# Optimization experiments

Measured on AMD Instinct MI355X. Metric: run time of the kernel, lower is better.

The kernel has to match this reference:

```python
import jax, jax.numpy as jnp
import numpy as np

N = 100000
E = 1600000
IN_CH = 128
HID = 16
HEADS = 4
OUT_CH = 2
EDGE_DIM = 3
NEG_SLOPE = 0.2


def gat_layer(x, src, dst, e_feat, W, att_src, att_dst, We, att_edge, bias, H, C, concat):
    # x: [N, Fin] -> projected [N, H, C]
    xs = (x @ W).reshape(-1, H, C)
    a_src = jnp.sum(xs * att_src, axis=-1)          # [N, H]
    a_dst = jnp.sum(xs * att_dst, axis=-1)          # [N, H]
    ee = (e_feat @ We).reshape(-1, H, C)            # [E, H, C]
    a_edge = jnp.sum(ee * att_edge, axis=-1)        # [E, H]
    alpha = a_src[src] + a_dst[dst] + a_edge        # [E, H]
    alpha = jax.nn.leaky_relu(alpha, NEG_SLOPE)
    # segment softmax over incoming edges of each dst node
    seg_max = jax.ops.segment_max(alpha, dst, num_segments=N)
    alpha = jnp.exp(alpha - seg_max[dst])
    seg_sum = jax.ops.segment_sum(alpha, dst, num_segments=N)
    alpha = alpha / (seg_sum[dst] + 1e-16)
    # weighted message aggregation
    msg = xs[src] * alpha[:, :, None]               # [E, H, C]
    out = jax.ops.segment_sum(msg, dst, num_segments=N)  # [N, H, C]
    out = out.reshape(-1, H * C) if concat else out.mean(axis=1)
    return out + bias


def setup_inputs() -> dict:
    key = jax.random.key(0)
    ks = jax.random.split(key, 24)
    g = lambda i, shape, scale=0.1: jax.random.normal(ks[i], shape, dtype=jnp.float32) * scale
    inp = {
        "x": jax.random.normal(ks[0], (N, IN_CH), dtype=jnp.float32),
        "edge_index": jax.random.randint(ks[1], (2, E), 0, N, dtype=jnp.int32),
        "edge_feat": jax.random.normal(ks[2], (E, EDGE_DIM), dtype=jnp.float32),
        # edge MLP
        "Em1": g(3, (EDGE_DIM, EDGE_DIM)), "eb1": g(4, (EDGE_DIM,)),
        "Em2": g(5, (EDGE_DIM, EDGE_DIM)), "eb2": g(6, (EDGE_DIM,)),
        # conv1: in -> HID per head, HEADS heads, concat
        "W1": g(7, (IN_CH, HEADS * HID)),
        "as1": g(8, (HEADS, HID)), "ad1": g(9, (HEADS, HID)),
        "We1": g(10, (EDGE_DIM, HEADS * HID)), "ae1": g(11, (HEADS, HID)),
        "b1": g(12, (HEADS * HID,)),
        # conv2: HEADS*HID -> OUT_CH, 1 head, no concat
        "W2": g(13, (HEADS * HID, OUT_CH)),
        "as2": g(14, (1, OUT_CH)), "ad2": g(15, (1, OUT_CH)),
        "We2": g(16, (EDGE_DIM, OUT_CH)), "ae2": g(17, (1, OUT_CH)),
        "b2": g(18, (OUT_CH,)),
    }
    return inp


def reference(x, edge_index, edge_feat,
              Em1, eb1, Em2, eb2,
              W1, as1, ad1, We1, ae1, b1,
              W2, as2, ad2, We2, ae2, b2):
    src, dst = edge_index[0], edge_index[1]
    # edge MLP: Linear -> ReLU -> Linear
    e = jax.nn.relu(edge_feat @ Em1 + eb1) @ Em2 + eb2
    # dropout layers are identity in eval mode
    h = gat_layer(x, src, dst, e, W1, as1, ad1, We1, ae1, b1, HEADS, HID, concat=True)
    h = jax.nn.elu(h)
    out = gat_layer(h, src, dst, e, W2, as2, ad2, We2, ae2, b2, 1, OUT_CH, concat=False)
    return out
```

## Files before the change

### kernel.cpp

```cpp
#include <hip/hip_runtime.h>
#include <hip/hip_fp16.h>
#include <math.h>
#include <stdint.h>

#define NEG_SLOPE 0.2f
#define SCAN_TILE 2048

__device__ __forceinline__ float leaky(float a) { return a > 0.f ? a : NEG_SLOPE * a; }

__global__ __launch_bounds__(256) void k_pw(const int* __restrict__ dst, int* __restrict__ deg,
                                            int* __restrict__ pw, int E,
                                            const float* __restrict__ We1, const float* __restrict__ ae1,
                                            const float* __restrict__ We2, const float* __restrict__ ae2,
                                            float* __restrict__ cw) {
    if (blockIdx.x == 0 && threadIdx.x == 0) {
        for (int i = 0; i < 3; i++)
            for (int h = 0; h < 4; h++) {
                float s = 0.f;
                for (int m = 0; m < 16; m++) s += We1[i*64 + h*16 + m] * ae1[h*16 + m];
                cw[i*4 + h] = s;
            }
        for (int i = 0; i < 3; i++) cw[12 + i] = We2[i*2]*ae2[0] + We2[i*2+1]*ae2[1];
    }
    int base = (blockIdx.x * blockDim.x + threadIdx.x) * 4;
    if (base >= E) return;
    if (base + 3 < E) {
        int4 dv = *reinterpret_cast<const int4*>(&dst[base]);
        int4 pv;
        pv.x = atomicAdd(&deg[dv.x], 1);
        pv.y = atomicAdd(&deg[dv.y], 1);
        pv.z = atomicAdd(&deg[dv.z], 1);
        pv.w = atomicAdd(&deg[dv.w], 1);
        *reinterpret_cast<int4*>(&pw[base]) = pv;
    } else {
        for (int i = base; i < E; i++) pw[i] = atomicAdd(&deg[dst[i]], 1);
    }
}

__global__ __launch_bounds__(256) void k_scan_partial(const int* __restrict__ deg, int* __restrict__ tsum, int N) {
    __shared__ int sh[256];
    int b = blockIdx.x, t = threadIdx.x;
    int base = b * SCAN_TILE + t * 8;
    int s = 0;
    #pragma unroll
    for (int i = 0; i < 8; i++) { int idx = base + i; s += (idx < N) ? deg[idx] : 0; }
    sh[t] = s; __syncthreads();
    for (int o = 128; o > 0; o >>= 1) { if (t < o) sh[t] += sh[t + o]; __syncthreads(); }
    if (t == 0) tsum[b] = sh[0];
}

__global__ void k_scan_tsum(const int* __restrict__ tsum, int* __restrict__ toff,
                            int* __restrict__ rowptr, int nb, int N) {
    if (threadIdx.x == 0 && blockIdx.x == 0) {
        int run = 0;
        for (int i = 0; i < nb; i++) { toff[i] = run; run += tsum[i]; }
        rowptr[N] = run;
    }
}

__global__ __launch_bounds__(256) void k_scan_final(const int* __restrict__ deg, const int* __restrict__ toff,
        int* __restrict__ rowptr, int* __restrict__ cmbi, int N) {
    __shared__ int sh[256];
    int b = blockIdx.x, t = threadIdx.x;
    int base = b * SCAN_TILE + t * 8;
    int v[8]; int s = 0;
    #pragma unroll
    for (int i = 0; i < 8; i++) { int idx = base + i; v[i] = (idx < N) ? deg[idx] : 0; s += v[i]; }
    sh[t] = s; __syncthreads();
    for (int o = 1; o < 256; o <<= 1) {
        int u = (t >= o) ? sh[t - o] : 0;
        __syncthreads();
        sh[t] += u;
        __syncthreads();
    }
    int run = sh[t] - s + toff[b];
    #pragma unroll
    for (int i = 0; i < 8; i++) {
        int idx = base + i;
        if (idx < N) { rowptr[idx] = run; cmbi[(size_t)idx*8 + 4] = run; run += v[i]; }
    }
}

__global__ __launch_bounds__(256) void k_proj1(const float* __restrict__ x, const float* __restrict__ W1,
        const float* __restrict__ as1, const float* __restrict__ ad1,
        __half* __restrict__ xs1h, float* __restrict__ as1v, float* __restrict__ cmbf, int N) {
    __shared__ float xr[32][128];
    int tid = threadIdx.x;
    int wave = tid >> 6, lane = tid & 63;
    int nbase = blockIdx.x * 32;
    if (nbase + 32 <= N) {
        const float4* x4 = reinterpret_cast<const float4*>(x + (size_t)nbase * 128);
        #pragma unroll
        for (int i = 0; i < 4; i++) {
            int idx = tid + i * 256;
            reinterpret_cast<float4*>(&xr[0][0])[idx] = x4[idx];
        }
    } else {
        for (int i = 0; i < 16; i++) {
            int flat = tid + i * 256;
            int row = flat >> 7, col = flat & 127;
            int n = nbase + row; if (n >= N) n = N - 1;
            xr[row][col] = x[(size_t)n * 128 + col];
        }
    }
    __syncthreads();
    int cc = lane & 15, kk = lane >> 4;
    int nw = wave * 8;
    const float4* W4 = reinterpret_cast<const float4*>(W1);
    float4 acc[8];
    #pragma unroll
    for (int m = 0; m < 8; m++) acc[m] = make_float4(0.f, 0.f, 0.f, 0.f);
    #pragma unroll 4
    for (int k = kk; k < 128; k += 4) {
        float4 wv = W4[k * 16 + cc];
        #pragma unroll
        for (int m = 0; m < 8; m++) {
            float xv = xr[nw + m][k];
            acc[m].x = fmaf(xv, wv.x, acc[m].x);
            acc[m].y = fmaf(xv, wv.y, acc[m].y);
            acc[m].z = fmaf(xv, wv.z, acc[m].z);
            acc[m].w = fmaf(xv, wv.w, acc[m].w);
        }
    }
    float a_s0 = as1[4*cc], a_s1 = as1[4*cc+1], a_s2 = as1[4*cc+2], a_s3 = as1[4*cc+3];
    float a_d0 = ad1[4*cc], a_d1 = ad1[4*cc+1], a_d2 = ad1[4*cc+2], a_d3 = ad1[4*cc+3];
    #pragma unroll
    for (int m = 0; m < 8; m++) {
        float4 a = acc[m];
        a.x += __shfl_xor(a.x, 16, 64); a.y += __shfl_xor(a.y, 16, 64);
        a.z += __shfl_xor(a.z, 16, 64); a.w += __shfl_xor(a.w, 16, 64);
        a.x += __shfl_xor(a.x, 32, 64); a.y += __shfl_xor(a.y, 32, 64);
        a.z += __shfl_xor(a.z, 32, 64); a.w += __shfl_xor(a.w, 32, 64);
        float ps = a.x*a_s0 + a.y*a_s1 + a.z*a_s2 + a.w*a_s3;
        float pd = a.x*a_d0 + a.y*a_d1 + a.z*a_d2 + a.w*a_d3;
        ps += __shfl_xor(ps, 1, 64); ps += __shfl_xor(ps, 2, 64);
        pd += __shfl_xor(pd, 1, 64); pd += __shfl_xor(pd, 2, 64);
        if (kk == 0) {
            int n = nbase + nw + m; if (n >= N) n = N - 1;
            __half2 h01 = __halves2half2(__float2half_rn(a.x), __float2half_rn(a.y));
            __half2 h23 = __halves2half2(__float2half_rn(a.z), __float2half_rn(a.w));
            uint2 st;
            st.x = *reinterpret_cast<unsigned*>(&h01);
            st.y = *reinterpret_cast<unsigned*>(&h23);
            *reinterpret_cast<uint2*>(&xs1h[(size_t)n*64 + 4*cc]) = st;
            if ((cc & 3) == 0) {
                int h = cc >> 2;
                as1v[n*4 + h] = ps;
                cmbf[(size_t)n*8 + h] = pd;
            }
        }
    }
}

__global__ __launch_bounds__(256) void k_payload(const float* __restrict__ ef,
                       const float* __restrict__ Em1, const float* __restrict__ eb1,
                       const float* __restrict__ Em2, const float* __restrict__ eb2,
                       const float* __restrict__ cw,
                       const int* __restrict__ src, const int* __restrict__ dst,
                       const int* __restrict__ pw,
                       const float4* __restrict__ as1v4,
                       const float* __restrict__ cmbf, const int* __restrict__ cmbi,
                       uint4* __restrict__ csr_pk, int E) {
    int base = (blockIdx.x * blockDim.x + threadIdx.x) * 4;
    if (base >= E) return;
    int cnt = min(4, E - base);

    float f[4][3]; int sv[4], dv[4], pv[4];
    if (cnt == 4) {
        const float4* ef4 = reinterpret_cast<const float4*>(ef);
        float4 a = ef4[base*3/4 + 0], b = ef4[base*3/4 + 1], c = ef4[base*3/4 + 2];
        f[0][0]=a.x; f[0][1]=a.y; f[0][2]=a.z;
        f[1][0]=a.w; f[1][1]=b.x; f[1][2]=b.y;
        f[2][0]=b.z; f[2][1]=b.w; f[2][2]=c.x;
        f[3][0]=c.y; f[3][1]=c.z; f[3][2]=c.w;
        int4 s4 = *reinterpret_cast<const int4*>(&src[base]);
        int4 d4 = *reinterpret_cast<const int4*>(&dst[base]);
        int4 p4 = *reinterpret_cast<const int4*>(&pw[base]);
        sv[0]=s4.x; sv[1]=s4.y; sv[2]=s4.z; sv[3]=s4.w;
        dv[0]=d4.x; dv[1]=d4.y; dv[2]=d4.z; dv[3]=d4.w;
        pv[0]=p4.x; pv[1]=p4.y; pv[2]=p4.z; pv[3]=p4.w;
    } else {
        for (int i = 0; i < cnt; i++) {
            f[i][0]=ef[(base+i)*3+0]; f[i][1]=ef[(base+i)*3+1]; f[i][2]=ef[(base+i)*3+2];
            sv[i]=src[base+i]; dv[i]=dst[base+i]; pv[i]=pw[base+i];
        }
    }

    #pragma unroll
    for (int i = 0; i < 4; i++) {
        if (i >= cnt) break;
        float f0=f[i][0], f1=f[i][1], f2=f[i][2];
        float t0 = fmaxf(f0*Em1[0]+f1*Em1[3]+f2*Em1[6]+eb1[0], 0.f);
        float t1 = fmaxf(f0*Em1[1]+f1*Em1[4]+f2*Em1[7]+eb1[1], 0.f);
        float t2 = fmaxf(f0*Em1[2]+f1*Em1[5]+f2*Em1[8]+eb1[2], 0.f);
        float u0 = t0*Em2[0]+t1*Em2[3]+t2*Em2[6]+eb2[0];
        float u1 = t0*Em2[1]+t1*Em2[4]+t2*Em2[7]+eb2[1];
        float u2 = t0*Em2[2]+t1*Em2[5]+t2*Em2[8]+eb2[2];
        int s = sv[i], d = dv[i];
        float4 av = as1v4[s];
        float4 bv = *reinterpret_cast<const float4*>(&cmbf[(size_t)d*8]);
        int rp = cmbi[(size_t)d*8 + 4];
        float w0 = __expf(leaky(av.x + bv.x + u0*cw[0] + u1*cw[4] + u2*cw[8]));
        float w1 = __expf(leaky(av.y + bv.y + u0*cw[1] + u1*cw[5] + u2*cw[9]));
        float w2 = __expf(leaky(av.z + bv.z + u0*cw[2] + u1*cw[6] + u2*cw[10]));
        float w3 = __expf(leaky(av.w + bv.w + u0*cw[3] + u1*cw[7] + u2*cw[11]));
        float e2 = u0*cw[12] + u1*cw[13] + u2*cw[14];
        __half2 lo = __halves2half2(__float2half_rn(w0), __float2half_rn(w1));
        __half2 hi = __halves2half2(__float2half_rn(w2), __float2half_rn(w3));
        uint4 pki;
        pki.x = (unsigned)s;
        pki.y = *reinterpret_cast<unsigned*>(&lo);
        pki.z = *reinterpret_cast<unsigned*>(&hi);
        pki.w = *reinterpret_cast<unsigned*>(&e2);
        csr_pk[rp + pv[i]] = pki;
    }
}

__global__ __launch_bounds__(256) void k_gat1(
        const int* __restrict__ rowptr, const uint4* __restrict__ csr_pk,
        const __half* __restrict__ xs1h,
        const float* __restrict__ b1, const float* __restrict__ W2,
        const float* __restrict__ as2, const float* __restrict__ ad2,
        float2* __restrict__ pk2, float* __restrict__ ad2v, int N) {
    int wave = threadIdx.x >> 6, lane = threadIdx.x & 63;
    int d = blockIdx.x * 4 + wave;
    if (d >= N) return;
    int beg = rowptr[d], end = rowptr[d+1];
    int jj = lane >> 2, hh = lane & 3;
    int k = lane, hk = lane >> 4;
    float smacc = 0.f, acc = 0.f;
    for (int off = beg; off < end; off += 16) {
        int j = off + jj;
        float w = 0.f; int s = 0;
        if (j < end) {
            uint4 p = csr_pk[j];
            s = (int)p.x;
            unsigned wb = (hh < 2) ? p.y : p.z;
            __half2 h2 = *reinterpret_cast<__half2*>(&wb);
            w = (hh & 1) ? __high2float(h2) : __low2float(h2);
        }
        smacc += w;
        if (end - off >= 16) {
            #pragma unroll
            for (int t = 0; t < 16; ++t) {
                float wt = __shfl(w, t*4 + hk, 64);
                int st   = __shfl(s, t*4, 64);
                acc = fmaf(wt, __half2float(xs1h[(size_t)st*64 + k]), acc);
            }
        } else {
            int lim = end - off;
            for (int t = 0; t < lim; ++t) {
                float wt = __shfl(w, t*4 + hk, 64);
                int st   = __shfl(s, t*4, 64);
                acc = fmaf(wt, __half2float(xs1h[(size_t)st*64 + k]), acc);
            }
        }
    }
    smacc += __shfl_xor(smacc, 4, 64);
    smacc += __shfl_xor(smacc, 8, 64);
    smacc += __shfl_xor(smacc, 16, 64);
    smacc += __shfl_xor(smacc, 32, 64);
    float sm = __shfl(smacc, hk, 64);
    float h = acc / (sm + 1e-16f);
    float v = h + b1[k];
    v = v > 0.f ? v : expm1f(v);
    float p0 = v * W2[k*2 + 0], p1 = v * W2[k*2 + 1];
    #pragma unroll
    for (int o = 32; o >= 1; o >>= 1) { p0 += __shfl_xor(p0,o,64); p1 += __shfl_xor(p1,o,64); }
    if (lane == 0) {
        float2 q;
        q.x = p0*as2[0] + p1*as2[1];
        __half2 xv = __halves2half2(__float2half_rn(p0), __float2half_rn(p1));
        q.y = *reinterpret_cast<float*>(&xv);
        pk2[d] = q;
        ad2v[d] = p0*ad2[0] + p1*ad2[1];
    }
}

__global__ __launch_bounds__(256) void k_gat2(
        const int* __restrict__ rowptr, const uint4* __restrict__ csr_pk,
        const float2* __restrict__ pk2, const float* __restrict__ ad2v,
        const float* __restrict__ b2, float* __restrict__ out, int N) {
    int t = blockIdx.x * blockDim.x + threadIdx.x;
    int d = t >> 4, j16 = t & 15;
    if (d >= N) return;
    int beg = rowptr[d], end = rowptr[d+1];
    float add = ad2v[d];
    float sm = 0.f, p0 = 0.f, p1 = 0.f;
    for (int off = beg; off < end; off += 16) {
        int j = off + j16;
        if (j < end) {
            uint4 p = csr_pk[j];
            int s = (int)p.x;
            float ea2 = *reinterpret_cast<float*>(&p.w);
            float2 q = pk2[s];
            float w = __expf(leaky(q.x + add + ea2));
            __half2 xv = *reinterpret_cast<__half2*>(&q.y);
            p0 = fmaf(w, __low2float(xv), p0);
            p1 = fmaf(w, __high2float(xv), p1);
            sm += w;
        }
    }
    #pragma unroll
    for (int o = 1; o < 16; o <<= 1) {
        sm += __shfl_xor(sm, o, 16);
        p0 += __shfl_xor(p0, o, 16);
        p1 += __shfl_xor(p1, o, 16);
    }
    if (j16 == 0) {
        float inv = 1.f / (sm + 1e-16f);
        out[d*2+0] = p0*inv + b2[0];
        out[d*2+1] = p1*inv + b2[1];
    }
}

extern "C" void kernel_launch(void* const* d_in, const int* in_sizes, int n_in,
                              void* d_out, int out_size, void* d_ws, size_t ws_size,
                              hipStream_t stream) {
    const float* x   = (const float*)d_in[0];
    const int*   ei  = (const int*)d_in[1];
    const float* ef  = (const float*)d_in[2];
    const float* Em1 = (const float*)d_in[3];
    const float* eb1 = (const float*)d_in[4];
    const float* Em2 = (const float*)d_in[5];
    const float* eb2 = (const float*)d_in[6];
    const float* W1  = (const float*)d_in[7];
    const float* as1 = (const float*)d_in[8];
    const float* ad1 = (const float*)d_in[9];
    const float* We1 = (const float*)d_in[10];
    const float* ae1 = (const float*)d_in[11];
    const float* b1  = (const float*)d_in[12];
    const float* W2  = (const float*)d_in[13];
    const float* as2 = (const float*)d_in[14];
    const float* ad2 = (const float*)d_in[15];
    const float* We2 = (const float*)d_in[16];
    const float* ae2 = (const float*)d_in[17];
    const float* b2  = (const float*)d_in[18];

    const int N = in_sizes[0] / 128;
    const int E = in_sizes[1] / 2;
    const int* srcp = ei;
    const int* dstp = ei + E;

    uintptr_t w = (uintptr_t)d_ws;
    auto alloc = [&](size_t bytes) -> void* {
        uintptr_t p = w; w += (bytes + 255) & ~(size_t)255; return (void*)p;
    };
    const int nb = (N + SCAN_TILE - 1) / SCAN_TILE;
    int*    deg     = (int*)alloc((size_t)N * sizeof(int));
    int*    rowptr  = (int*)alloc(((size_t)N + 1) * sizeof(int));
    int*    tsum    = (int*)alloc((size_t)nb * sizeof(int));
    int*    toff    = (int*)alloc((size_t)(nb + 1) * sizeof(int));
    float*  cw      = (float*)alloc(16 * sizeof(float));
    int*    pw      = (int*)alloc((size_t)E * sizeof(int));
    uint4*  csr_pk  = (uint4*)alloc((size_t)E * sizeof(uint4));
    __half* xs1h    = (__half*)alloc((size_t)N * 64 * sizeof(__half));
    float*  as1v    = (float*)alloc((size_t)N * 4 * sizeof(float));
    float*  cmb     = (float*)alloc((size_t)N * 8 * sizeof(float));
    float2* pk2     = (float2*)alloc((size_t)N * sizeof(float2));
    float*  ad2v    = (float*)alloc((size_t)N * sizeof(float));

    const int B = 256;

    hipMemsetAsync(deg, 0, (size_t)N * sizeof(int), stream);
    k_pw<<<(E/4+B-1)/B + 1, B, 0, stream>>>(dstp, deg, pw, E, We1, ae1, We2, ae2, cw);
    k_scan_partial<<<nb, 256, 0, stream>>>(deg, tsum, N);
    k_scan_tsum<<<1, 64, 0, stream>>>(tsum, toff, rowptr, nb, N);
    k_scan_final<<<nb, 256, 0, stream>>>(deg, toff, rowptr, (int*)cmb, N);
    k_proj1<<<(N+31)/32, 256, 0, stream>>>(x, W1, as1, ad1, xs1h, as1v, cmb, N);
    k_payload<<<(E/4+B-1)/B + 1, B, 0, stream>>>(ef, Em1, eb1, Em2, eb2, cw,
                                                 srcp, dstp, pw, (const float4*)as1v,
                                                 cmb, (const int*)cmb, csr_pk, E);
    k_gat1<<<(N+3)/4, 256, 0, stream>>>(rowptr, csr_pk, xs1h, b1, W2, as2, ad2, pk2, ad2v, N);
    k_gat2<<<(N*16+B-1)/B, B, 0, stream>>>(rowptr, csr_pk, pk2, ad2v, b2, (float*)d_out, N);
}
```

Baseline: 276.0 us.

## Restructure GAT layer-1 aggregation to process four edges per wave with vectorized gathers

The layer-1 aggregation kernel is remapped so each wave splits into four 16-lane groups. Each group handles a different edge, and each lane gathers four fp16 channels with an 8-byte load, where before every lane loaded a single channel per edge. Partial sums are then combined across the groups with cross-lane shuffles, and the softmax denominator is reduced within 16-lane segments. This is meant to cut per-edge load instruction count and serial shuffle overhead, and it adds a launch-bounds occupancy hint. The cost is extra shuffles per chunk and higher register pressure.

```diff
diff --git a/kernel.cpp b/kernel.cpp
--- a/kernel.cpp
+++ b/kernel.cpp
@@ -7,6 +7,7 @@
 #define SCAN_TILE 2048
 
 __device__ __forceinline__ float leaky(float a) { return a > 0.f ? a : NEG_SLOPE * a; }
+__device__ __forceinline__ __half2 u2h2(unsigned u) { return *reinterpret_cast<__half2*>(&u); }
 
 __global__ __launch_bounds__(256) void k_pw(const int* __restrict__ dst, int* __restrict__ deg,
                                             int* __restrict__ pw, int E,
@@ -216,7 +217,7 @@
     }
 }
 
-__global__ __launch_bounds__(256) void k_gat1(
+__global__ __launch_bounds__(256, 4) void k_gat1(
         const int* __restrict__ rowptr, const uint4* __restrict__ csr_pk,
         const __half* __restrict__ xs1h,
         const float* __restrict__ b1, const float* __restrict__ W2,
@@ -226,47 +227,78 @@
     int d = blockIdx.x * 4 + wave;
     if (d >= N) return;
     int beg = rowptr[d], end = rowptr[d+1];
-    int jj = lane >> 2, hh = lane & 3;
-    int k = lane, hk = lane >> 4;
-    float smacc = 0.f, acc = 0.f;
+    int cg = lane & 15, e4 = lane >> 4;
+    int hh = cg >> 2;
+    const __half* xbase = xs1h + 4 * cg;
+    float4 acc = make_float4(0.f, 0.f, 0.f, 0.f);
+    float4 wv  = make_float4(0.f, 0.f, 0.f, 0.f);
     for (int off = beg; off < end; off += 16) {
-        int j = off + jj;
-        float w = 0.f; int s = 0;
-        if (j < end) {
-            uint4 p = csr_pk[j];
-            s = (int)p.x;
-            unsigned wb = (hh < 2) ? p.y : p.z;
-            __half2 h2 = *reinterpret_cast<__half2*>(&wb);
-            w = (hh & 1) ? __high2float(h2) : __low2float(h2);
-        }
-        smacc += w;
-        if (end - off >= 16) {
-            #pragma unroll
-            for (int t = 0; t < 16; ++t) {
-                float wt = __shfl(w, t*4 + hk, 64);
-                int st   = __shfl(s, t*4, 64);
-                acc = fmaf(wt, __half2float(xs1h[(size_t)st*64 + k]), acc);
-            }
-        } else {
-            int lim = end - off;
-            for (int t = 0; t < lim; ++t) {
-                float wt = __shfl(w, t*4 + hk, 64);
-                int st   = __shfl(s, t*4, 64);
-                acc = fmaf(wt, __half2float(xs1h[(size_t)st*64 + k]), acc);
-            }
-        }
-    }
-    smacc += __shfl_xor(smacc, 4, 64);
-    smacc += __shfl_xor(smacc, 8, 64);
-    smacc += __shfl_xor(smacc, 16, 64);
-    smacc += __shfl_xor(smacc, 32, 64);
-    float sm = __shfl(smacc, hk, 64);
-    float h = acc / (sm + 1e-16f);
-    float v = h + b1[k];
-    v = v > 0.f ? v : expm1f(v);
-    float p0 = v * W2[k*2 + 0], p1 = v * W2[k*2 + 1];
-    #pragma unroll
-    for (int o = 32; o >= 1; o >>= 1) { p0 += __shfl_xor(p0,o,64); p1 += __shfl_xor(p1,o,64); }
+        int j = off + cg;
+        uint4 p = make_uint4(0u, 0u, 0u, 0u);
+        if (j < end) p = csr_pk[j];
+        int si = (int)p.x;
+        __half2 wl = u2h2(p.y), whp = u2h2(p.z);
+        wv.x += __low2float(wl);  wv.y += __high2float(wl);
+        wv.z += __low2float(whp); wv.w += __high2float(whp);
+        int st0, st1, st2, st3; float wt0, wt1, wt2, wt3;
+        {
+            int sl0 = 0*4 + e4, sl1 = 1*4 + e4, sl2 = 2*4 + e4, sl3 = 3*4 + e4;
+            st0 = __shfl(si, sl0, 16); st1 = __shfl(si, sl1, 16);
+            st2 = __shfl(si, sl2, 16); st3 = __shfl(si, sl3, 16);
+            unsigned y0 = __shfl(p.y, sl0, 16), z0 = __shfl(p.z, sl0, 16);
+            unsigned y1 = __shfl(p.y, sl1, 16), z1 = __shfl(p.z, sl1, 16);
+            unsigned y2 = __shfl(p.y, sl2, 16), z2 = __shfl(p.z, sl2, 16);
+            unsigned y3 = __shfl(p.y, sl3, 16), z3 = __shfl(p.z, sl3, 16);
+            unsigned q0 = (hh < 2) ? y0 : z0;
+            unsigned q1 = (hh < 2) ? y1 : z1;
+            unsigned q2 = (hh < 2) ? y2 : z2;
+            unsigned q3 = (hh < 2) ? y3 : z3;
+            wt0 = (hh & 1) ? __high2float(u2h2(q0)) : __low2float(u2h2(q0));
+            wt1 = (hh & 1) ? __high2float(u2h2(q1)) : __low2float(u2h2(q1));
+            wt2 = (hh & 1) ? __high2float(u2h2(q2)) : __low2float(u2h2(q2));
+            wt3 = (hh & 1) ? __high2float(u2h2(q3)) : __low2float(u2h2(q3));
+        }
+        uint2 g0 = *reinterpret_cast<const uint2*>(xbase + ((size_t)st0 << 6));
+        uint2 g1 = *reinterpret_cast<const uint2*>(xbase + ((size_t)st1 << 6));
+        uint2 g2 = *reinterpret_cast<const uint2*>(xbase + ((size_t)st2 << 6));
+        uint2 g3 = *reinterpret_cast<const uint2*>(xbase + ((size_t)st3 << 6));
+        __half2 a, b;
+        a = u2h2(g0.x); b = u2h2(g0.y);
+        acc.x = fmaf(wt0, __low2float(a), acc.x); acc.y = fmaf(wt0, __high2float(a), acc.y);
+        acc.z = fmaf(wt0, __low2float(b), acc.z); acc.w = fmaf(wt0, __high2float(b), acc.w);
+        a = u2h2(g1.x); b = u2h2(g1.y);
+        acc.x = fmaf(wt1, __low2float(a), acc.x); acc.y = fmaf(wt1, __high2float(a), acc.y);
+        acc.z = fmaf(wt1, __low2float(b), acc.z); acc.w = fmaf(wt1, __high2float(b), acc.w);
+        a = u2h2(g2.x); b = u2h2(g2.y);
+        acc.x = fmaf(wt2, __low2float(a), acc.x); acc.y = fmaf(wt2, __high2float(a), acc.y);
+        acc.z = fmaf(wt2, __low2float(b), acc.z); acc.w = fmaf(wt2, __high2float(b), acc.w);
+        a = u2h2(g3.x); b = u2h2(g3.y);
+        acc.x = fmaf(wt3, __low2float(a), acc.x); acc.y = fmaf(wt3, __high2float(a), acc.y);
+        acc.z = fmaf(wt3, __low2float(b), acc.z); acc.w = fmaf(wt3, __high2float(b), acc.w);
+    }
+    acc.x += __shfl_xor(acc.x, 16, 64); acc.y += __shfl_xor(acc.y, 16, 64);
+    acc.z += __shfl_xor(acc.z, 16, 64); acc.w += __shfl_xor(acc.w, 16, 64);
+    acc.x += __shfl_xor(acc.x, 32, 64); acc.y += __shfl_xor(acc.y, 32, 64);
+    acc.z += __shfl_xor(acc.z, 32, 64); acc.w += __shfl_xor(acc.w, 32, 64);
+    #pragma unroll
+    for (int o = 1; o <= 8; o <<= 1) {
+        wv.x += __shfl_xor(wv.x, o, 16); wv.y += __shfl_xor(wv.y, o, 16);
+        wv.z += __shfl_xor(wv.z, o, 16); wv.w += __shfl_xor(wv.w, o, 16);
+    }
+    float sm = (hh == 0) ? wv.x : (hh == 1) ? wv.y : (hh == 2) ? wv.z : wv.w;
+    float inv = 1.f / (sm + 1e-16f);
+    float v0 = acc.x * inv + b1[4*cg + 0];
+    float v1 = acc.y * inv + b1[4*cg + 1];
+    float v2 = acc.z * inv + b1[4*cg + 2];
+    float v3 = acc.w * inv + b1[4*cg + 3];
+    v0 = v0 > 0.f ? v0 : expm1f(v0);
+    v1 = v1 > 0.f ? v1 : expm1f(v1);
+    v2 = v2 > 0.f ? v2 : expm1f(v2);
+    v3 = v3 > 0.f ? v3 : expm1f(v3);
+    float p0 = v0*W2[(4*cg+0)*2] + v1*W2[(4*cg+1)*2] + v2*W2[(4*cg+2)*2] + v3*W2[(4*cg+3)*2];
+    float p1 = v0*W2[(4*cg+0)*2+1] + v1*W2[(4*cg+1)*2+1] + v2*W2[(4*cg+2)*2+1] + v3*W2[(4*cg+3)*2+1];
+    #pragma unroll
+    for (int o = 1; o <= 8; o <<= 1) { p0 += __shfl_xor(p0, o, 16); p1 += __shfl_xor(p1, o, 16); }
     if (lane == 0) {
         float2 q;
         q.x = p0*as2[0] + p1*as2[1];
```

Measured after the change: 251.5 us. 8.9% less time.
